# Optimization experiments

Measured on AMD Instinct MI355X. Metric: run time of the kernel, lower is better.

## Reference

```python
import jax, jax.numpy as jnp
from jax import lax
import numpy as np

# Model hyper-parameters (from init_kwargs)
B = 4
POINT_NUM = 32768
SKP_NUM = 512
ISK_NUM = 2
K1 = 32                       # skp_neighbor_num
K2 = int(K1 * SKP_NUM * 4 / POINT_NUM)   # = 2, as computed in __init__
RADIUS_SCALING = 1.5
SPHERE_N = 128                # points per sphere template


def _fibonacci_sphere(n):
    i = np.arange(n, dtype=np.float64) + 0.5
    phi = np.arccos(1.0 - 2.0 * i / n)
    theta = np.pi * (1.0 + 5.0 ** 0.5) * i
    return np.stack([np.cos(theta) * np.sin(phi),
                     np.sin(theta) * np.sin(phi),
                     np.cos(phi)], axis=-1).astype(np.float32)


def setup_inputs() -> dict:
    key = jax.random.key(0)
    xyz = jax.random.normal(key, (B, POINT_NUM, 3), dtype=jnp.float32)
    sphere_template = jnp.asarray(_fibonacci_sphere(SPHERE_N))  # [S,3] unit sphere
    return {"xyz": xyz, "sphere_template": sphere_template}


def _fps(xyz, n):
    """Iterative furthest point sampling. xyz: [B,N,3] -> indices [B,n] int32."""
    b, N, _ = xyz.shape
    dist0 = jnp.full((b, N), 1e10, dtype=xyz.dtype)
    last0 = jnp.zeros((b,), dtype=jnp.int32)

    def step(carry, _):
        dist, last = carry
        lp = jnp.take_along_axis(xyz, last[:, None, None], axis=1)  # [B,1,3]
        d = jnp.sum((xyz - lp) ** 2, axis=-1)                        # [B,N]
        dist = jnp.minimum(dist, d)
        nxt = jnp.argmax(dist, axis=-1).astype(jnp.int32)
        return (dist, nxt), last

    (_, _), idxs = lax.scan(step, (dist0, last0), None, length=n)
    return idxs.T  # [B,n]


def _pairwise_sqdist(centers, pts):
    # [B,M,N] squared distances
    c2 = jnp.sum(centers ** 2, axis=-1)[:, :, None]
    p2 = jnp.sum(pts ** 2, axis=-1)[:, None, :]
    cp = jnp.einsum('bmd,bnd->bmn', centers, pts)
    return c2 + p2 - 2.0 * cp


def _sklnz(centers, pts, k):
    """SkeletonizationBlock: move each center to the mean of its k nearest
    points in pts; radius = mean distance to those neighbors."""
    d2 = _pairwise_sqdist(centers, pts)          # [B,M,N]
    neg, idx = lax.top_k(-d2, k)                 # [B,M,k]
    nb = jax.vmap(lambda x, i: x[i])(pts, idx)   # [B,M,k,3]
    new_centers = jnp.mean(nb, axis=2)
    radius = jnp.mean(jnp.sqrt(jnp.clip(-neg, 0.0)), axis=2)  # [B,M]
    return new_centers, radius


def _forward(xyz, sphere_template):
    # Stage 1: FPS to 4*skp_num seeds, then iterative skeletonization
    ids = _fps(xyz, SKP_NUM * 4)                               # [B,4*skp]
    centers = jnp.take_along_axis(xyz, ids[:, :, None], axis=1)
    radius = None
    for _ in range(ISK_NUM):
        centers, radius = _sklnz(centers, xyz, K1)
    # Stage 2: FPS on intermediate skeleton down to skp_num
    xyz2 = centers
    ids2 = _fps(xyz2, SKP_NUM)                                 # [B,skp]
    centers = jnp.take_along_axis(xyz2, ids2[:, :, None], axis=1)
    radius = jnp.take_along_axis(radius, ids2, axis=1)
    for _ in range(ISK_NUM):
        centers, _radius = _sklnz(centers, xyz2, K2)
    radius = (radius + _radius) * RADIUS_SCALING               # [B,skp]
    # Sphere reconstruction: template scaled by radius, translated to centers
    sphere_points = centers[:, :, None, :] + radius[:, :, None, None] * sphere_template[None, None]
    return centers, sphere_points, radius


def reference(xyz, sphere_template):
    return _forward(xyz, sphere_template)
```

## Files before the change

kernel.cpp:

```cpp
#include <hip/hip_runtime.h>
#include <cstdint>

#define BATCH 4
#define NPTS  32768
#define QN    8192
#define SKP   512
#define M1    (SKP*4)
#define KA    32
#define KB    2
#define SPHN  128

__device__ __forceinline__ float sqdist(float px, float py, float pz,
                                        float cx, float cy, float cz) {
  float dx = px - cx, dy = py - cy, dz = pz - cz;
  return __fadd_rn(__fadd_rn(__fmul_rn(dx, dx), __fmul_rn(dy, dy)),
                   __fmul_rn(dz, dz));
}
__device__ __forceinline__ float d2gram(float px, float py, float pz,
                                        float qx, float qy, float qz, float q2) {
  float p2 = __fadd_rn(__fadd_rn(__fmul_rn(px, px), __fmul_rn(py, py)),
                       __fmul_rn(pz, pz));
  float cp = __fadd_rn(__fadd_rn(__fmul_rn(qx, px), __fmul_rn(qy, py)),
                       __fmul_rn(qz, pz));
  return __fsub_rn(__fadd_rn(q2, p2), __fadd_rn(cp, cp));
}

__device__ __forceinline__ unsigned long long shfl_xor_u64(unsigned long long v, int off) {
  int lo = __shfl_xor((int)(unsigned)v, off);
  int hi = __shfl_xor((int)(unsigned)(v >> 32), off);
  return ((unsigned long long)(unsigned)hi << 32) | (unsigned)lo;
}
__device__ __forceinline__ unsigned long long shfl_u64(unsigned long long v, int src) {
  int lo = __shfl((int)(unsigned)v, src);
  int hi = __shfl((int)(unsigned)(v >> 32), src);
  return ((unsigned long long)(unsigned)hi << 32) | (unsigned)lo;
}
__device__ __forceinline__ unsigned long long umax64(unsigned long long a, unsigned long long b) {
  return a > b ? a : b;
}
__device__ __forceinline__ unsigned long long umin64(unsigned long long a, unsigned long long b) {
  return a < b ? a : b;
}
__device__ __forceinline__ void ins3(unsigned long long& k1, unsigned long long& k2,
                                     unsigned long long& k3, unsigned long long v) {
  k3 = umax64(k3, umin64(k2, v));
  k2 = umax64(k2, umin64(k1, v));
  k1 = umax64(k1, v);
}

__global__ __launch_bounds__(1024)
void fps1_kernel(const float* __restrict__ xyz, int* __restrict__ ids,
                 unsigned long long* __restrict__ sync)
{
  int blk = blockIdx.x;
  int b = blk >> 2, sub = blk & 3;
  const float* X = xyz + (size_t)b * NPTS * 3;
  ids += (size_t)b * M1;
  int tid = threadIdx.x, lane = tid & 63, wave = tid >> 6;
  int base = sub * QN;

  __shared__ float2 xysh[QN];
  __shared__ unsigned long long s_w[16][3];
  __shared__ float s_pivc[32][3];
  __shared__ int s_J;

  float zr[8], dist[8];
#pragma unroll
  for (int j = 0; j < 8; ++j) {
    int pl = tid + 1024 * j;
    int pg = base + pl;
    xysh[pl] = make_float2(X[3*pg], X[3*pg+1]);
    zr[j] = X[3*pg+2];
    dist[j] = 1e10f;
  }
  if (tid == 0) {
    s_pivc[0][0] = X[0]; s_pivc[0][1] = X[1]; s_pivc[0][2] = X[2];
    if (sub == 0) ids[0] = 0;
  }
  __syncthreads();

  int it = 1, J = 1, rc = 1;

  while (it < M1) {
    for (int jp0 = 0; jp0 < J; jp0 += 4) {
      float pxa[4], pya[4], pza[4];
#pragma unroll
      for (int l = 0; l < 4; ++l) {
        int jj = jp0 + l; jj = (jj < J) ? jj : jp0;
        pxa[l] = s_pivc[jj][0]; pya[l] = s_pivc[jj][1]; pza[l] = s_pivc[jj][2];
      }
#pragma unroll
      for (int j = 0; j < 8; ++j) {
        int pl = tid + 1024 * j;
        float2 c2 = xysh[pl];
        float dd = dist[j];
#pragma unroll
        for (int l = 0; l < 4; ++l)
          dd = fminf(dd, sqdist(c2.x, c2.y, zr[j], pxa[l], pya[l], pza[l]));
        dist[j] = dd;
      }
    }
    unsigned long long k1 = 0, k2 = 0, k3 = 0;
#pragma unroll
    for (int j = 0; j < 8; ++j) {
      int pg = base + tid + 1024 * j;
      unsigned long long key =
          ((unsigned long long)__float_as_uint(dist[j]) << 15) |
          (unsigned)(0x7FFF - pg);
      ins3(k1, k2, k3, key);
    }
#pragma unroll
    for (int off = 32; off > 0; off >>= 1) {
      unsigned long long o1 = shfl_xor_u64(k1, off);
      unsigned long long o2 = shfl_xor_u64(k2, off);
      unsigned long long o3 = shfl_xor_u64(k3, off);
      ins3(k1, k2, k3, o1);
      ins3(k1, k2, k3, o2);
      ins3(k1, k2, k3, o3);
    }
    if (lane == 0) { s_w[wave][0] = k1; s_w[wave][1] = k2; s_w[wave][2] = k3; }
    __syncthreads();
    if (wave == 0) {
      unsigned long long fb = (lane < 16) ? s_w[lane][2] : 0;
#pragma unroll
      for (int off = 8; off > 0; off >>= 1) {
        unsigned long long o = shfl_xor_u64(fb, off);
        if (o > fb) fb = o;
      }
      fb = shfl_u64(fb, 0);
      unsigned tag = (unsigned)rc;
      int par = rc & 1;
      int sbase = ((b * 2 + par) * 4 + sub) * 40;
      unsigned long long mycand = 0;
      if (lane < 16)      mycand = s_w[lane][0];
      else if (lane < 32) mycand = s_w[lane - 16][1];
      if (lane < 32)
        __hip_atomic_store(&sync[sbase + lane], (mycand << 12) | tag,
                           __ATOMIC_RELAXED, __HIP_MEMORY_SCOPE_AGENT);
      if (lane == 32)
        __hip_atomic_store(&sync[sbase + 32], (fb << 12) | tag,
                           __ATOMIC_RELAXED, __HIP_MEMORY_SCOPE_AGENT);
      int rel = (sub + (lane >> 4)) & 3;
      int cb = ((b * 2 + par) * 4 + rel) * 40;
      int c0s = cb + (lane & 15);
      int c1s = cb + 16 + (lane & 15);
      int fsl = ((b * 2 + par) * 4 + ((sub + lane) & 3)) * 40 + 32;
      unsigned long long ck0 = 0, ck1 = 0, flr = 0;
      bool n0 = true, n1 = true, nf = (lane < 4);
      while (__any(n0 || n1 || nf)) {
        if (n0) {
          unsigned long long v = __hip_atomic_load(&sync[c0s],
                                  __ATOMIC_RELAXED, __HIP_MEMORY_SCOPE_AGENT);
          if ((unsigned)(v & 0xFFFu) == tag) { ck0 = v >> 12; n0 = false; }
        }
        if (n1) {
          unsigned long long v = __hip_atomic_load(&sync[c1s],
                                  __ATOMIC_RELAXED, __HIP_MEMORY_SCOPE_AGENT);
          if ((unsigned)(v & 0xFFFu) == tag) { ck1 = v >> 12; n1 = false; }
        }
        if (nf) {
          unsigned long long v = __hip_atomic_load(&sync[fsl],
                                  __ATOMIC_RELAXED, __HIP_MEMORY_SCOPE_AGENT);
          if ((unsigned)(v & 0xFFFu) == tag) { flr = v >> 12; nf = false; }
        }
      }
      unsigned long long f = umax64(umax64(shfl_u64(flr, 0), shfl_u64(flr, 1)),
                                    umax64(shfl_u64(flr, 2), shfl_u64(flr, 3)));
      int ci0 = 0x7FFF - (int)(ck0 & 0x7FFFu);
      int ci1 = 0x7FFF - (int)(ck1 & 0x7FFFu);
      float cx0 = X[3*ci0], cy0 = X[3*ci0+1], cz0 = X[3*ci0+2];
      float cx1 = X[3*ci1], cy1 = X[3*ci1+1], cz1 = X[3*ci1+2];
      int Jn = 0;
      while (it + Jn < M1 && Jn < 32) {
        unsigned long long mk = umax64(ck0, ck1);
#pragma unroll
        for (int off = 32; off > 0; off >>= 1) {
          unsigned long long o = shfl_xor_u64(mk, off);
          if (o > mk) mk = o;
        }
        if (!(mk > f)) break;
        unsigned long long b0 = __ballot(ck0 == mk);
        float px, py, pz;
        if (b0) {
          int wl = __ffsll((long long)b0) - 1;
          px = __shfl(cx0, wl); py = __shfl(cy0, wl); pz = __shfl(cz0, wl);
        } else {
          unsigned long long b1 = __ballot(ck1 == mk);
          int wl = __ffsll((long long)b1) - 1;
          px = __shfl(cx1, wl); py = __shfl(cy1, wl); pz = __shfl(cz1, wl);
        }
        if (lane == 0) {
          s_pivc[Jn][0] = px; s_pivc[Jn][1] = py; s_pivc[Jn][2] = pz;
          if (sub == 0) ids[it + Jn] = 0x7FFF - (int)(mk & 0x7FFFu);
        }
        float d0 = sqdist(cx0, cy0, cz0, px, py, pz);
        float n0v = fminf(__uint_as_float((unsigned)(ck0 >> 15)), d0);
        ck0 = ((unsigned long long)__float_as_uint(n0v) << 15) | (ck0 & 0x7FFFu);
        float d1 = sqdist(cx1, cy1, cz1, px, py, pz);
        float n1v = fminf(__uint_as_float((unsigned)(ck1 >> 15)), d1);
        ck1 = ((unsigned long long)__float_as_uint(n1v) << 15) | (ck1 & 0x7FFFu);
        ++Jn;
      }
      if (lane == 0) s_J = Jn;
    }
    __syncthreads();
    J = s_J;
    it += J;
    rc += 1;
  }
}

__global__ __launch_bounds__(1024)
void fps2_kernel(const float4* __restrict__ pts, int* __restrict__ ids)
{
  int b = blockIdx.x;
  pts += (size_t)b * M1;
  ids += (size_t)b * SKP;
  int tid = threadIdx.x, lane = tid & 63, wave = tid >> 6;

  __shared__ float4 pl[M1];
  __shared__ unsigned long long s_w[16][3];
  __shared__ float s_pivc[16][3];
  __shared__ int s_J;

  float4 f0 = pts[tid], f1 = pts[tid + 1024];
  pl[tid] = f0; pl[tid + 1024] = f1;
  float dist0 = 1e10f, dist1 = 1e10f;
  if (tid == 0) {
    ids[0] = 0;
    s_pivc[0][0] = f0.x; s_pivc[0][1] = f0.y; s_pivc[0][2] = f0.z;
  }
  __syncthreads();

  int it = 1, J = 1;

  while (it < SKP) {
    for (int jp0 = 0; jp0 < J; jp0 += 4) {
      float pxa[4], pya[4], pza[4];
#pragma unroll
      for (int l = 0; l < 4; ++l) {
        int jj = jp0 + l; jj = (jj < J) ? jj : jp0;
        pxa[l] = s_pivc[jj][0]; pya[l] = s_pivc[jj][1]; pza[l] = s_pivc[jj][2];
      }
#pragma unroll
      for (int l = 0; l < 4; ++l) {
        dist0 = fminf(dist0, sqdist(f0.x, f0.y, f0.z, pxa[l], pya[l], pza[l]));
        dist1 = fminf(dist1, sqdist(f1.x, f1.y, f1.z, pxa[l], pya[l], pza[l]));
      }
    }
    unsigned long long k1, k2 = 0, k3 = 0;
    k1 = ((unsigned long long)__float_as_uint(dist0) << 15) | (unsigned)(0x7FFF - tid);
    {
      unsigned long long key =
          ((unsigned long long)__float_as_uint(dist1) << 15) | (unsigned)(0x7FFF - (tid + 1024));
      ins3(k1, k2, k3, key);
    }
#pragma unroll
    for (int off = 32; off > 0; off >>= 1) {
      unsigned long long o1 = shfl_xor_u64(k1, off);
      unsigned long long o2 = shfl_xor_u64(k2, off);
      unsigned long long o3 = shfl_xor_u64(k3, off);
      ins3(k1, k2, k3, o1);
      ins3(k1, k2, k3, o2);
      ins3(k1, k2, k3, o3);
    }
    if (lane == 0) { s_w[wave][0] = k1; s_w[wave][1] = k2; s_w[wave][2] = k3; }
    __syncthreads();
    if (wave == 0) {
      unsigned long long fb = (lane < 16) ? s_w[lane][2] : 0;
#pragma unroll
      for (int off = 8; off > 0; off >>= 1) {
        unsigned long long o = shfl_xor_u64(fb, off);
        if (o > fb) fb = o;
      }
      unsigned long long f = shfl_u64(fb, 0);
      unsigned long long ck = 0;
      if (lane < 16)      ck = s_w[lane][0];
      else if (lane < 32) ck = s_w[lane - 16][1];
      int ci = (0x7FFF - (int)(ck & 0x7FFFu)) & (M1 - 1);
      float4 c = pl[ci];
      int Jn = 0;
      while (it + Jn < SKP && Jn < 16) {
        unsigned long long mk = ck;
#pragma unroll
        for (int off = 32; off > 0; off >>= 1) {
          unsigned long long o = shfl_xor_u64(mk, off);
          if (o > mk) mk = o;
        }
        if (!(mk > f)) break;
        unsigned long long ball = __ballot(ck == mk);
        int wl = __ffsll((long long)ball) - 1;
        float px = __shfl(c.x, wl), py = __shfl(c.y, wl), pz = __shfl(c.z, wl);
        if (lane == 0) {
          s_pivc[Jn][0] = px; s_pivc[Jn][1] = py; s_pivc[Jn][2] = pz;
          ids[it + Jn] = 0x7FFF - (int)(mk & 0x7FFFu);
        }
        float d = sqdist(c.x, c.y, c.z, px, py, pz);
        float nv = fminf(__uint_as_float((unsigned)(ck >> 15)), d);
        ck = ((unsigned long long)__float_as_uint(nv) << 15) | (ck & 0x7FFFu);
        ++Jn;
      }
      if (lane == 0) s_J = Jn;
    }
    __syncthreads();
    J = s_J;
    it += J;
  }
}

template<int K, int KL, int N, bool S3>
__global__ __launch_bounds__(256)
void sklnz_kernel(const float4* __restrict__ queries,
                  const void*   __restrict__ ptsv,
                  float4* __restrict__ outc,
                  float*  __restrict__ outr,
                  int M)
{
  const int CH = N / 64;
  int wave = threadIdx.x >> 6, lane = threadIdx.x & 63;
  int qid = blockIdx.x * 4 + wave;
  int b = qid / M;
  const float*  P3 = (const float*)ptsv + (size_t)b * N * 3;
  const float4* P4 = (const float4*)ptsv + (size_t)b * N;
  float4 q = queries[qid];
  float q2 = __fadd_rn(__fadd_rn(__fmul_rn(q.x, q.x), __fmul_rn(q.y, q.y)),
                       __fmul_rn(q.z, q.z));

  __shared__ float heads[4][64][K + 1];

  float a[KL];
#pragma unroll
  for (int s = 0; s < KL; ++s) a[s] = 3.0e38f;
  for (int j = 0; j < CH; ++j) {
    int p = lane + 64 * j;
    float px, py, pz;
    if (S3) { px = P3[3*p]; py = P3[3*p+1]; pz = P3[3*p+2]; }
    else    { float4 f = P4[p]; px = f.x; py = f.y; pz = f.z; }
    float d = d2gram(px, py, pz, q.x, q.y, q.z, q2);
#pragma unroll
    for (int s = KL - 1; s > 0; --s) a[s] = fminf(a[s], fmaxf(a[s-1], d));
    a[0] = fminf(a[0], d);
  }
#pragma unroll
  for (int s = 0; s < KL; ++s) heads[wave][lane][s] = a[s];
  heads[wave][lane][KL] = 3.1e38f;
  int h = 0; float t = 0.f;
  for (int r = 0; r < K; ++r) {
    float mv = heads[wave][lane][h];
    int   ml = lane;
#pragma unroll
    for (int off = 32; off > 0; off >>= 1) {
      float ov = __shfl_xor(mv, off);
      int   ol = __shfl_xor(ml, off);
      if (ov < mv || (ov == mv && ol < ml)) { mv = ov; ml = ol; }
    }
    t = mv;
    if (ml == lane) h++;
  }

  float sx = 0.f, sy = 0.f, sz = 0.f, sr = 0.f;
  int cl = 0;
  int myNext = 0x7fffffff;
  for (int j = 0; j < CH; ++j) {
    int p = lane + 64 * j;
    float px, py, pz;
    if (S3) { px = P3[3*p]; py = P3[3*p+1]; pz = P3[3*p+2]; }
    else    { float4 f = P4[p]; px = f.x; py = f.y; pz = f.z; }
    float d = d2gram(px, py, pz, q.x, q.y, q.z, q2);
    if (d < t) { sx += px; sy += py; sz += pz; sr += sqrtf(fmaxf(d, 0.f)); cl++; }
    else if (d == t && myNext == 0x7fffffff) myNext = p;
  }
  int ctot = cl;
#pragma unroll
  for (int off = 32; off > 0; off >>= 1) ctot += __shfl_xor(ctot, off);

  if constexpr (KL < K) {
    if (ctot >= K) {
      float a2[K];
#pragma unroll
      for (int s = 0; s < K; ++s) a2[s] = 3.0e38f;
      for (int j = 0; j < CH; ++j) {
        int p = lane + 64 * j;
        float px, py, pz;
        if (S3) { px = P3[3*p]; py = P3[3*p+1]; pz = P3[3*p+2]; }
        else    { float4 f = P4[p]; px = f.x; py = f.y; pz = f.z; }
        float d = d2gram(px, py, pz, q.x, q.y, q.z, q2);
#pragma unroll
        for (int s = K - 1; s > 0; --s) a2[s] = fminf(a2[s], fmaxf(a2[s-1], d));
        a2[0] = fminf(a2[0], d);
      }
#pragma unroll
      for (int s = 0; s < K; ++s) heads[wave][lane][s] = a2[s];
      heads[wave][lane][K] = 3.1e38f;
      h = 0;
      for (int r = 0; r < K; ++r) {
        float mv = heads[wave][lane][h];
        int   ml = lane;
#pragma unroll
        for (int off = 32; off > 0; off >>= 1) {
          float ov = __shfl_xor(mv, off);
          int   ol = __shfl_xor(ml, off);
          if (ov < mv || (ov == mv && ol < ml)) { mv = ov; ml = ol; }
        }
        t = mv;
        if (ml == lane) h++;
      }
      sx = sy = sz = sr = 0.f; cl = 0; myNext = 0x7fffffff;
      for (int j = 0; j < CH; ++j) {
        int p = lane + 64 * j;
        float px, py, pz;
        if (S3) { px = P3[3*p]; py = P3[3*p+1]; pz = P3[3*p+2]; }
        else    { float4 f = P4[p]; px = f.x; py = f.y; pz = f.z; }
        float d = d2gram(px, py, pz, q.x, q.y, q.z, q2);
        if (d < t) { sx += px; sy += py; sz += pz; sr += sqrtf(fmaxf(d, 0.f)); cl++; }
        else if (d == t && myNext == 0x7fffffff) myNext = p;
      }
      ctot = cl;
#pragma unroll
      for (int off = 32; off > 0; off >>= 1) ctot += __shfl_xor(ctot, off);
    }
  }

  int need = K - ctot;
  float rt = sqrtf(fmaxf(t, 0.f));

  for (int e = 0; e < need; ++e) {
    int mn = myNext;
#pragma unroll
    for (int off = 32; off > 0; off >>= 1) mn = min(mn, __shfl_xor(mn, off));
    if (myNext == mn) {
      float px, py, pz;
      if (S3) { px = P3[3*mn]; py = P3[3*mn+1]; pz = P3[3*mn+2]; }
      else    { float4 f = P4[mn]; px = f.x; py = f.y; pz = f.z; }
      sx += px; sy += py; sz += pz; sr += rt;
      int nx = 0x7fffffff;
      for (int j = (mn - lane) / 64 + 1; j < CH; ++j) {
        int p = lane + 64 * j;
        float ux, uy, uz;
        if (S3) { ux = P3[3*p]; uy = P3[3*p+1]; uz = P3[3*p+2]; }
        else    { float4 f = P4[p]; ux = f.x; uy = f.y; uz = f.z; }
        float d = d2gram(ux, uy, uz, q.x, q.y, q.z, q2);
        if (d == t) { nx = p; break; }
      }
      myNext = nx;
    }
  }

#pragma unroll
  for (int off = 32; off > 0; off >>= 1) {
    sx += __shfl_xor(sx, off);
    sy += __shfl_xor(sy, off);
    sz += __shfl_xor(sz, off);
    sr += __shfl_xor(sr, off);
  }
  if (lane == 0) {
    const float inv = 1.0f / (float)K;
    outc[qid] = make_float4(sx * inv, sy * inv, sz * inv, 0.f);
    outr[qid] = sr * inv;
  }
}

__global__ void gather1_kernel(const float* __restrict__ xyz,
                               const int* __restrict__ ids,
                               float4* __restrict__ cen)
{
  int g = blockIdx.x * 256 + threadIdx.x;
  if (g >= BATCH * M1) return;
  int b = g / M1;
  size_t base = ((size_t)b * NPTS + ids[g]) * 3;
  cen[g] = make_float4(xyz[base], xyz[base+1], xyz[base+2], 0.f);
}

__global__ void gather2_kernel(const float4* __restrict__ cen4,
                               const float* __restrict__ rad1,
                               const int* __restrict__ ids2,
                               float4* __restrict__ cen2,
                               float* __restrict__ radg)
{
  int g = blockIdx.x * 256 + threadIdx.x;
  if (g >= BATCH * SKP) return;
  int b = g / SKP;
  int p = ids2[g];
  cen2[g] = cen4[(size_t)b * M1 + p];
  radg[g] = rad1[(size_t)b * M1 + p];
}

__global__ void finalize_kernel(const float4* __restrict__ cen,
                                const float* __restrict__ radg,
                                const float* __restrict__ rad2,
                                const float* __restrict__ tmpl,
                                float* __restrict__ out)
{
  int g = blockIdx.x * 256 + threadIdx.x;
  int s = g >> 7;
  int j = g & 127;
  float4 c = cen[s];
  float r = __fmul_rn(__fadd_rn(radg[s], rad2[s]), 1.5f);
  float tx = tmpl[3*j], ty = tmpl[3*j+1], tz = tmpl[3*j+2];
  float* sp = out + BATCH * SKP * 3;
  sp[3*g]     = __fadd_rn(c.x, __fmul_rn(r, tx));
  sp[3*g + 1] = __fadd_rn(c.y, __fmul_rn(r, ty));
  sp[3*g + 2] = __fadd_rn(c.z, __fmul_rn(r, tz));
  if (j == 0) {
    out[3*s] = c.x; out[3*s+1] = c.y; out[3*s+2] = c.z;
    out[BATCH*SKP*3 + BATCH*SKP*SPHN*3 + s] = r;
  }
}

extern "C" void kernel_launch(void* const* d_in, const int* in_sizes, int n_in,
                              void* d_out, int out_size, void* d_ws, size_t ws_size,
                              hipStream_t stream)
{
  const float* xyz  = (const float*)d_in[0];
  const float* tmpl = (const float*)d_in[1];
  float* out = (float*)d_out;
  char* ws = (char*)d_ws;

  int*    ids1  = (int*)   (ws + 0);
  float4* cen4a = (float4*)(ws + 32768);
  float4* cen4b = (float4*)(ws + 163840);
  float*  rad1  = (float*) (ws + 294912);
  int*    ids2  = (int*)   (ws + 327680);
  float4* cen2a = (float4*)(ws + 335872);
  float4* cen2b = (float4*)(ws + 368640);
  float*  radg  = (float*) (ws + 401408);
  float*  rad2  = (float*) (ws + 409600);
  unsigned long long* sync = (unsigned long long*)(ws + 417792);

  fps1_kernel<<<BATCH * 4, 1024, 0, stream>>>(xyz, ids1, sync);
  gather1_kernel<<<(BATCH * M1 + 255) / 256, 256, 0, stream>>>(xyz, ids1, cen4a);
  sklnz_kernel<KA, 8, NPTS, true><<<BATCH * M1 / 4, 256, 0, stream>>>(cen4a, xyz, cen4b, rad1, M1);
  sklnz_kernel<KA, 8, NPTS, true><<<BATCH * M1 / 4, 256, 0, stream>>>(cen4b, xyz, cen4a, rad1, M1);
  fps2_kernel<<<BATCH, 1024, 0, stream>>>(cen4a, ids2);
  gather2_kernel<<<(BATCH * SKP + 255) / 256, 256, 0, stream>>>(cen4a, rad1, ids2, cen2a, radg);
  sklnz_kernel<KB, KB, M1, false><<<BATCH * SKP / 4, 256, 0, stream>>>(cen2a, cen4a, cen2b, rad2, SKP);
  sklnz_kernel<KB, KB, M1, false><<<BATCH * SKP / 4, 256, 0, stream>>>(cen2b, cen4a, cen2a, rad2, SKP);
  finalize_kernel<<<BATCH * SKP * SPHN / 256, 256, 0, stream>>>(cen2a, radg, rad2, tmpl, out);
}
```

Baseline: 4.079 ms.

## Widen FPS candidate batches, fuse gather into FPS, vectorize kNN point loads

The multi-block FPS kernel now keeps four candidates per wave instead of three. Each round it pulls 48 candidates from the four sub-blocks and can accept up to 48 pivots, which cuts the number of cross-block sync rounds. FPS writes the center coordinates directly, so the separate gather kernel is dropped. The skeletonization kernel loads xyz as three float4s per four points instead of scalar strided loads, and its first-pass local top-K is lowered from 8 to 4. The smaller per-lane top-K may trigger the slower fallback rescan path more often, and the tie-handling index logic was rewritten along with it.

```diff
diff --git a/kernel.cpp b/kernel.cpp
--- a/kernel.cpp
+++ b/kernel.cpp
@@ -47,21 +47,29 @@
   k2 = umax64(k2, umin64(k1, v));
   k1 = umax64(k1, v);
 }
+__device__ __forceinline__ void ins4(unsigned long long& k1, unsigned long long& k2,
+                                     unsigned long long& k3, unsigned long long& k4,
+                                     unsigned long long v) {
+  k4 = umax64(k4, umin64(k3, v));
+  k3 = umax64(k3, umin64(k2, v));
+  k2 = umax64(k2, umin64(k1, v));
+  k1 = umax64(k1, v);
+}
 
 __global__ __launch_bounds__(1024)
-void fps1_kernel(const float* __restrict__ xyz, int* __restrict__ ids,
+void fps1_kernel(const float* __restrict__ xyz, float4* __restrict__ cen4a,
                  unsigned long long* __restrict__ sync)
 {
   int blk = blockIdx.x;
   int b = blk >> 2, sub = blk & 3;
   const float* X = xyz + (size_t)b * NPTS * 3;
-  ids += (size_t)b * M1;
+  cen4a += (size_t)b * M1;
   int tid = threadIdx.x, lane = tid & 63, wave = tid >> 6;
   int base = sub * QN;
 
   __shared__ float2 xysh[QN];
-  __shared__ unsigned long long s_w[16][3];
-  __shared__ float s_pivc[32][3];
+  __shared__ unsigned long long s_w[16][4];
+  __shared__ float s_pivc[48][3];
   __shared__ int s_J;
 
   float zr[8], dist[8];
@@ -75,7 +83,7 @@
   }
   if (tid == 0) {
     s_pivc[0][0] = X[0]; s_pivc[0][1] = X[1]; s_pivc[0][2] = X[2];
-    if (sub == 0) ids[0] = 0;
+    if (sub == 0) cen4a[0] = make_float4(X[0], X[1], X[2], 0.f);
   }
   __syncthreads();
 
@@ -100,28 +108,32 @@
         dist[j] = dd;
       }
     }
-    unsigned long long k1 = 0, k2 = 0, k3 = 0;
+    unsigned long long k1 = 0, k2 = 0, k3 = 0, k4 = 0;
 #pragma unroll
     for (int j = 0; j < 8; ++j) {
       int pg = base + tid + 1024 * j;
       unsigned long long key =
           ((unsigned long long)__float_as_uint(dist[j]) << 15) |
           (unsigned)(0x7FFF - pg);
-      ins3(k1, k2, k3, key);
+      ins4(k1, k2, k3, k4, key);
     }
 #pragma unroll
     for (int off = 32; off > 0; off >>= 1) {
       unsigned long long o1 = shfl_xor_u64(k1, off);
       unsigned long long o2 = shfl_xor_u64(k2, off);
       unsigned long long o3 = shfl_xor_u64(k3, off);
-      ins3(k1, k2, k3, o1);
-      ins3(k1, k2, k3, o2);
-      ins3(k1, k2, k3, o3);
-    }
-    if (lane == 0) { s_w[wave][0] = k1; s_w[wave][1] = k2; s_w[wave][2] = k3; }
+      unsigned long long o4 = shfl_xor_u64(k4, off);
+      ins4(k1, k2, k3, k4, o1);
+      ins4(k1, k2, k3, k4, o2);
+      ins4(k1, k2, k3, k4, o3);
+      ins4(k1, k2, k3, k4, o4);
+    }
+    if (lane == 0) {
+      s_w[wave][0] = k1; s_w[wave][1] = k2; s_w[wave][2] = k3; s_w[wave][3] = k4;
+    }
     __syncthreads();
     if (wave == 0) {
-      unsigned long long fb = (lane < 16) ? s_w[lane][2] : 0;
+      unsigned long long fb = (lane < 16) ? s_w[lane][3] : 0;
 #pragma unroll
       for (int off = 8; off > 0; off >>= 1) {
         unsigned long long o = shfl_xor_u64(fb, off);
@@ -130,75 +142,81 @@
       fb = shfl_u64(fb, 0);
       unsigned tag = (unsigned)rc;
       int par = rc & 1;
-      int sbase = ((b * 2 + par) * 4 + sub) * 40;
-      unsigned long long mycand = 0;
-      if (lane < 16)      mycand = s_w[lane][0];
-      else if (lane < 32) mycand = s_w[lane - 16][1];
-      if (lane < 32)
-        __hip_atomic_store(&sync[sbase + lane], (mycand << 12) | tag,
+      int sbase = ((b * 2 + par) * 4 + sub) * 56;
+      if (lane < 48)
+        __hip_atomic_store(&sync[sbase + lane],
+                           (s_w[lane & 15][lane >> 4] << 12) | tag,
                            __ATOMIC_RELAXED, __HIP_MEMORY_SCOPE_AGENT);
-      if (lane == 32)
-        __hip_atomic_store(&sync[sbase + 32], (fb << 12) | tag,
+      if (lane == 48)
+        __hip_atomic_store(&sync[sbase + 48], (fb << 12) | tag,
                            __ATOMIC_RELAXED, __HIP_MEMORY_SCOPE_AGENT);
-      int rel = (sub + (lane >> 4)) & 3;
-      int cb = ((b * 2 + par) * 4 + rel) * 40;
-      int c0s = cb + (lane & 15);
-      int c1s = cb + 16 + (lane & 15);
-      int fsl = ((b * 2 + par) * 4 + ((sub + lane) & 3)) * 40 + 32;
-      unsigned long long ck0 = 0, ck1 = 0, flr = 0;
-      bool n0 = true, n1 = true, nf = (lane < 4);
-      while (__any(n0 || n1 || nf)) {
-        if (n0) {
-          unsigned long long v = __hip_atomic_load(&sync[c0s],
+      unsigned long long ck[3];
+      int slots[3]; bool need[3];
+#pragma unroll
+      for (int k = 0; k < 3; ++k) {
+        int q = lane + 64 * k;
+        int r = q / 48, s = q % 48;
+        if (r == 0) { ck[k] = s_w[s & 15][s >> 4]; need[k] = false; slots[k] = 0; }
+        else {
+          slots[k] = ((b * 2 + par) * 4 + ((sub + r) & 3)) * 56 + s;
+          need[k] = true; ck[k] = 0;
+        }
+      }
+      bool needf = (lane < 3);
+      int fslot = ((b * 2 + par) * 4 + ((sub + 1 + lane) & 3)) * 56 + 48;
+      unsigned long long flr = 0;
+      while (__any(need[0] || need[1] || need[2] || needf)) {
+#pragma unroll
+        for (int k = 0; k < 3; ++k) if (need[k]) {
+          unsigned long long v = __hip_atomic_load(&sync[slots[k]],
                                   __ATOMIC_RELAXED, __HIP_MEMORY_SCOPE_AGENT);
-          if ((unsigned)(v & 0xFFFu) == tag) { ck0 = v >> 12; n0 = false; }
-        }
-        if (n1) {
-          unsigned long long v = __hip_atomic_load(&sync[c1s],
+          if ((unsigned)(v & 0xFFFu) == tag) { ck[k] = v >> 12; need[k] = false; }
+        }
+        if (needf) {
+          unsigned long long v = __hip_atomic_load(&sync[fslot],
                                   __ATOMIC_RELAXED, __HIP_MEMORY_SCOPE_AGENT);
-          if ((unsigned)(v & 0xFFFu) == tag) { ck1 = v >> 12; n1 = false; }
-        }
-        if (nf) {
-          unsigned long long v = __hip_atomic_load(&sync[fsl],
-                                  __ATOMIC_RELAXED, __HIP_MEMORY_SCOPE_AGENT);
-          if ((unsigned)(v & 0xFFFu) == tag) { flr = v >> 12; nf = false; }
-        }
-      }
-      unsigned long long f = umax64(umax64(shfl_u64(flr, 0), shfl_u64(flr, 1)),
-                                    umax64(shfl_u64(flr, 2), shfl_u64(flr, 3)));
-      int ci0 = 0x7FFF - (int)(ck0 & 0x7FFFu);
-      int ci1 = 0x7FFF - (int)(ck1 & 0x7FFFu);
-      float cx0 = X[3*ci0], cy0 = X[3*ci0+1], cz0 = X[3*ci0+2];
-      float cx1 = X[3*ci1], cy1 = X[3*ci1+1], cz1 = X[3*ci1+2];
+          if ((unsigned)(v & 0xFFFu) == tag) { flr = v >> 12; needf = false; }
+        }
+      }
+      unsigned long long f = fb;
+      f = umax64(f, shfl_u64(flr, 0));
+      f = umax64(f, shfl_u64(flr, 1));
+      f = umax64(f, shfl_u64(flr, 2));
+      float cxx[3], cyy[3], czz[3];
+#pragma unroll
+      for (int k = 0; k < 3; ++k) {
+        int ci = 0x7FFF - (int)(ck[k] & 0x7FFFu);
+        cxx[k] = X[3*ci]; cyy[k] = X[3*ci+1]; czz[k] = X[3*ci+2];
+      }
       int Jn = 0;
-      while (it + Jn < M1 && Jn < 32) {
-        unsigned long long mk = umax64(ck0, ck1);
+      while (it + Jn < M1 && Jn < 48) {
+        unsigned long long mk = umax64(umax64(ck[0], ck[1]), ck[2]);
 #pragma unroll
         for (int off = 32; off > 0; off >>= 1) {
           unsigned long long o = shfl_xor_u64(mk, off);
           if (o > mk) mk = o;
         }
         if (!(mk > f)) break;
-        unsigned long long b0 = __ballot(ck0 == mk);
-        float px, py, pz;
-        if (b0) {
-          int wl = __ffsll((long long)b0) - 1;
-          px = __shfl(cx0, wl); py = __shfl(cy0, wl); pz = __shfl(cz0, wl);
-        } else {
-          unsigned long long b1 = __ballot(ck1 == mk);
-          int wl = __ffsll((long long)b1) - 1;
-          px = __shfl(cx1, wl); py = __shfl(cy1, wl); pz = __shfl(cz1, wl);
+        float px = 0.f, py = 0.f, pz = 0.f;
+#pragma unroll
+        for (int k = 0; k < 3; ++k) {
+          unsigned long long bb = __ballot(ck[k] == mk);
+          if (bb) {
+            int wl = __ffsll((long long)bb) - 1;
+            px = __shfl(cxx[k], wl); py = __shfl(cyy[k], wl); pz = __shfl(czz[k], wl);
+            break;
+          }
         }
         if (lane == 0) {
           s_pivc[Jn][0] = px; s_pivc[Jn][1] = py; s_pivc[Jn][2] = pz;
-          if (sub == 0) ids[it + Jn] = 0x7FFF - (int)(mk & 0x7FFFu);
-        }
-        float d0 = sqdist(cx0, cy0, cz0, px, py, pz);
-        float n0v = fminf(__uint_as_float((unsigned)(ck0 >> 15)), d0);
-        ck0 = ((unsigned long long)__float_as_uint(n0v) << 15) | (ck0 & 0x7FFFu);
-        float d1 = sqdist(cx1, cy1, cz1, px, py, pz);
-        float n1v = fminf(__uint_as_float((unsigned)(ck1 >> 15)), d1);
-        ck1 = ((unsigned long long)__float_as_uint(n1v) << 15) | (ck1 & 0x7FFFu);
+          if (sub == 0) cen4a[it + Jn] = make_float4(px, py, pz, 0.f);
+        }
+#pragma unroll
+        for (int k = 0; k < 3; ++k) {
+          float d = sqdist(cxx[k], cyy[k], czz[k], px, py, pz);
+          float nv = fminf(__uint_as_float((unsigned)(ck[k] >> 15)), d);
+          ck[k] = ((unsigned long long)__float_as_uint(nv) << 15) | (ck[k] & 0x7FFFu);
+        }
         ++Jn;
       }
       if (lane == 0) s_J = Jn;
@@ -317,11 +335,13 @@
                   int M)
 {
   const int CH = N / 64;
+  const int CHP = N / 256;
   int wave = threadIdx.x >> 6, lane = threadIdx.x & 63;
   int qid = blockIdx.x * 4 + wave;
   int b = qid / M;
   const float*  P3 = (const float*)ptsv + (size_t)b * N * 3;
   const float4* P4 = (const float4*)ptsv + (size_t)b * N;
+  const float4* P4p = (const float4*)P3;
   float4 q = queries[qid];
   float q2 = __fadd_rn(__fadd_rn(__fmul_rn(q.x, q.x), __fmul_rn(q.y, q.y)),
                        __fmul_rn(q.z, q.z));
@@ -331,15 +351,30 @@
   float a[KL];
 #pragma unroll
   for (int s = 0; s < KL; ++s) a[s] = 3.0e38f;
-  for (int j = 0; j < CH; ++j) {
-    int p = lane + 64 * j;
-    float px, py, pz;
-    if (S3) { px = P3[3*p]; py = P3[3*p+1]; pz = P3[3*p+2]; }
-    else    { float4 f = P4[p]; px = f.x; py = f.y; pz = f.z; }
-    float d = d2gram(px, py, pz, q.x, q.y, q.z, q2);
-#pragma unroll
-    for (int s = KL - 1; s > 0; --s) a[s] = fminf(a[s], fmaxf(a[s-1], d));
-    a[0] = fminf(a[0], d);
+  if constexpr (S3) {
+    for (int j = 0; j < CHP; ++j) {
+      int u = lane + 64 * j;
+      float4 A = P4p[3*u], B = P4p[3*u+1], C = P4p[3*u+2];
+      float ds[4];
+      ds[0] = d2gram(A.x, A.y, A.z, q.x, q.y, q.z, q2);
+      ds[1] = d2gram(A.w, B.x, B.y, q.x, q.y, q.z, q2);
+      ds[2] = d2gram(B.z, B.w, C.x, q.x, q.y, q.z, q2);
+      ds[3] = d2gram(C.y, C.z, C.w, q.x, q.y, q.z, q2);
+#pragma unroll
+      for (int e = 0; e < 4; ++e) {
+#pragma unroll
+        for (int s = KL - 1; s > 0; --s) a[s] = fminf(a[s], fmaxf(a[s-1], ds[e]));
+        a[0] = fminf(a[0], ds[e]);
+      }
+    }
+  } else {
+    for (int j = 0; j < CH; ++j) {
+      float4 f = P4[lane + 64 * j];
+      float d = d2gram(f.x, f.y, f.z, q.x, q.y, q.z, q2);
+#pragma unroll
+      for (int s = KL - 1; s > 0; --s) a[s] = fminf(a[s], fmaxf(a[s-1], d));
+      a[0] = fminf(a[0], d);
+    }
   }
 #pragma unroll
   for (int s = 0; s < KL; ++s) heads[wave][lane][s] = a[s];
@@ -361,14 +396,29 @@
   float sx = 0.f, sy = 0.f, sz = 0.f, sr = 0.f;
   int cl = 0;
   int myNext = 0x7fffffff;
-  for (int j = 0; j < CH; ++j) {
-    int p = lane + 64 * j;
-    float px, py, pz;
-    if (S3) { px = P3[3*p]; py = P3[3*p+1]; pz = P3[3*p+2]; }
-    else    { float4 f = P4[p]; px = f.x; py = f.y; pz = f.z; }
-    float d = d2gram(px, py, pz, q.x, q.y, q.z, q2);
-    if (d < t) { sx += px; sy += py; sz += pz; sr += sqrtf(fmaxf(d, 0.f)); cl++; }
-    else if (d == t && myNext == 0x7fffffff) myNext = p;
+  if constexpr (S3) {
+    for (int j = 0; j < CHP; ++j) {
+      int u = lane + 64 * j;
+      float4 A = P4p[3*u], B = P4p[3*u+1], C = P4p[3*u+2];
+      float pxs[4] = {A.x, A.w, B.z, C.y};
+      float pys[4] = {A.y, B.x, B.w, C.z};
+      float pzs[4] = {A.z, B.y, C.x, C.w};
+#pragma unroll
+      for (int e = 0; e < 4; ++e) {
+        float d = d2gram(pxs[e], pys[e], pzs[e], q.x, q.y, q.z, q2);
+        if (d < t) { sx += pxs[e]; sy += pys[e]; sz += pzs[e];
+                     sr += sqrtf(fmaxf(d, 0.f)); cl++; }
+        else if (d == t && myNext == 0x7fffffff) myNext = 4*u + e;
+      }
+    }
+  } else {
+    for (int j = 0; j < CH; ++j) {
+      int p = lane + 64 * j;
+      float4 f = P4[p];
+      float d = d2gram(f.x, f.y, f.z, q.x, q.y, q.z, q2);
+      if (d < t) { sx += f.x; sy += f.y; sz += f.z; sr += sqrtf(fmaxf(d, 0.f)); cl++; }
+      else if (d == t && myNext == 0x7fffffff) myNext = p;
+    }
   }
   int ctot = cl;
 #pragma unroll
@@ -379,15 +429,20 @@
       float a2[K];
 #pragma unroll
       for (int s = 0; s < K; ++s) a2[s] = 3.0e38f;
-      for (int j = 0; j < CH; ++j) {
-        int p = lane + 64 * j;
-        float px, py, pz;
-        if (S3) { px = P3[3*p]; py = P3[3*p+1]; pz = P3[3*p+2]; }
-        else    { float4 f = P4[p]; px = f.x; py = f.y; pz = f.z; }
-        float d = d2gram(px, py, pz, q.x, q.y, q.z, q2);
-#pragma unroll
-        for (int s = K - 1; s > 0; --s) a2[s] = fminf(a2[s], fmaxf(a2[s-1], d));
-        a2[0] = fminf(a2[0], d);
+      for (int j = 0; j < CHP; ++j) {
+        int u = lane + 64 * j;
+        float4 A = P4p[3*u], B = P4p[3*u+1], C = P4p[3*u+2];
+        float ds[4];
+        ds[0] = d2gram(A.x, A.y, A.z, q.x, q.y, q.z, q2);
+        ds[1] = d2gram(A.w, B.x, B.y, q.x, q.y, q.z, q2);
+        ds[2] = d2gram(B.z, B.w, C.x, q.x, q.y, q.z, q2);
+        ds[3] = d2gram(C.y, C.z, C.w, q.x, q.y, q.z, q2);
+#pragma unroll
+        for (int e = 0; e < 4; ++e) {
+#pragma unroll
+          for (int s = K - 1; s > 0; --s) a2[s] = fminf(a2[s], fmaxf(a2[s-1], ds[e]));
+          a2[0] = fminf(a2[0], ds[e]);
+        }
       }
 #pragma unroll
       for (int s = 0; s < K; ++s) heads[wave][lane][s] = a2[s];
@@ -406,14 +461,19 @@
         if (ml == lane) h++;
       }
       sx = sy = sz = sr = 0.f; cl = 0; myNext = 0x7fffffff;
-      for (int j = 0; j < CH; ++j) {
-        int p = lane + 64 * j;
-        float px, py, pz;
-        if (S3) { px = P3[3*p]; py = P3[3*p+1]; pz = P3[3*p+2]; }
-        else    { float4 f = P4[p]; px = f.x; py = f.y; pz = f.z; }
-        float d = d2gram(px, py, pz, q.x, q.y, q.z, q2);
-        if (d < t) { sx += px; sy += py; sz += pz; sr += sqrtf(fmaxf(d, 0.f)); cl++; }
-        else if (d == t && myNext == 0x7fffffff) myNext = p;
+      for (int j = 0; j < CHP; ++j) {
+        int u = lane + 64 * j;
+        float4 A = P4p[3*u], B = P4p[3*u+1], C = P4p[3*u+2];
+        float pxs[4] = {A.x, A.w, B.z, C.y};
+        float pys[4] = {A.y, B.x, B.w, C.z};
+        float pzs[4] = {A.z, B.y, C.x, C.w};
+#pragma unroll
+        for (int e = 0; e < 4; ++e) {
+          float d = d2gram(pxs[e], pys[e], pzs[e], q.x, q.y, q.z, q2);
+          if (d < t) { sx += pxs[e]; sy += pys[e]; sz += pzs[e];
+                       sr += sqrtf(fmaxf(d, 0.f)); cl++; }
+          else if (d == t && myNext == 0x7fffffff) myNext = 4*u + e;
+        }
       }
       ctot = cl;
 #pragma unroll
@@ -424,7 +484,7 @@
   int need = K - ctot;
   float rt = sqrtf(fmaxf(t, 0.f));
 
-  for (int e = 0; e < need; ++e) {
+  for (int e0 = 0; e0 < need; ++e0) {
     int mn = myNext;
 #pragma unroll
     for (int off = 32; off > 0; off >>= 1) mn = min(mn, __shfl_xor(mn, off));
@@ -434,13 +494,27 @@
       else    { float4 f = P4[mn]; px = f.x; py = f.y; pz = f.z; }
       sx += px; sy += py; sz += pz; sr += rt;
       int nx = 0x7fffffff;
-      for (int j = (mn - lane) / 64 + 1; j < CH; ++j) {
-        int p = lane + 64 * j;
-        float ux, uy, uz;
-        if (S3) { ux = P3[3*p]; uy = P3[3*p+1]; uz = P3[3*p+2]; }
-        else    { float4 f = P4[p]; ux = f.x; uy = f.y; uz = f.z; }
-        float d = d2gram(ux, uy, uz, q.x, q.y, q.z, q2);
-        if (d == t) { nx = p; break; }
+      if constexpr (S3) {
+        for (int j = ((mn >> 2) - lane) / 64; j < CHP && nx == 0x7fffffff; ++j) {
+          int u = lane + 64 * j;
+          float4 A = P4p[3*u], B = P4p[3*u+1], C = P4p[3*u+2];
+          float pxs[4] = {A.x, A.w, B.z, C.y};
+          float pys[4] = {A.y, B.x, B.w, C.z};
+          float pzs[4] = {A.z, B.y, C.x, C.w};
+#pragma unroll
+          for (int e = 0; e < 4; ++e) {
+            int p = 4*u + e;
+            float d = d2gram(pxs[e], pys[e], pzs[e], q.x, q.y, q.z, q2);
+            if (p > mn && d == t && nx == 0x7fffffff) nx = p;
+          }
+        }
+      } else {
+        for (int j = (mn - lane) / 64 + 1; j < CH && nx == 0x7fffffff; ++j) {
+          int p = lane + 64 * j;
+          float4 f = P4[p];
+          float d = d2gram(f.x, f.y, f.z, q.x, q.y, q.z, q2);
+          if (d == t) nx = p;
+        }
       }
       myNext = nx;
     }
@@ -458,17 +532,6 @@
     outc[qid] = make_float4(sx * inv, sy * inv, sz * inv, 0.f);
     outr[qid] = sr * inv;
   }
-}
-
-__global__ void gather1_kernel(const float* __restrict__ xyz,
-                               const int* __restrict__ ids,
-                               float4* __restrict__ cen)
-{
-  int g = blockIdx.x * 256 + threadIdx.x;
-  if (g >= BATCH * M1) return;
-  int b = g / M1;
-  size_t base = ((size_t)b * NPTS + ids[g]) * 3;
-  cen[g] = make_float4(xyz[base], xyz[base+1], xyz[base+2], 0.f);
 }
 
 __global__ void gather2_kernel(const float4* __restrict__ cen4,
@@ -516,7 +579,6 @@
   float* out = (float*)d_out;
   char* ws = (char*)d_ws;
 
-  int*    ids1  = (int*)   (ws + 0);
   float4* cen4a = (float4*)(ws + 32768);
   float4* cen4b = (float4*)(ws + 163840);
   float*  rad1  = (float*) (ws + 294912);
@@ -527,10 +589,9 @@
   float*  rad2  = (float*) (ws + 409600);
   unsigned long long* sync = (unsigned long long*)(ws + 417792);
 
-  fps1_kernel<<<BATCH * 4, 1024, 0, stream>>>(xyz, ids1, sync);
-  gather1_kernel<<<(BATCH * M1 + 255) / 256, 256, 0, stream>>>(xyz, ids1, cen4a);
-  sklnz_kernel<KA, 8, NPTS, true><<<BATCH * M1 / 4, 256, 0, stream>>>(cen4a, xyz, cen4b, rad1, M1);
-  sklnz_kernel<KA, 8, NPTS, true><<<BATCH * M1 / 4, 256, 0, stream>>>(cen4b, xyz, cen4a, rad1, M1);
+  fps1_kernel<<<BATCH * 4, 1024, 0, stream>>>(xyz, cen4a, sync);
+  sklnz_kernel<KA, 4, NPTS, true><<<BATCH * M1 / 4, 256, 0, stream>>>(cen4a, xyz, cen4b, rad1, M1);
+  sklnz_kernel<KA, 4, NPTS, true><<<BATCH * M1 / 4, 256, 0, stream>>>(cen4b, xyz, cen4a, rad1, M1);
   fps2_kernel<<<BATCH, 1024, 0, stream>>>(cen4a, ids2);
   gather2_kernel<<<(BATCH * SKP + 255) / 256, 256, 0, stream>>>(cen4a, rad1, ids2, cen2a, radg);
   sklnz_kernel<KB, KB, M1, false><<<BATCH * SKP / 4, 256, 0, stream>>>(cen2a, cen4a, cen2b, rad2, SKP);
```

Measured after the change: 4.029 ms. About the same (-1.2%).
